# Kernel optimization log

Hardware: AMD Instinct MI355X
Metric: run time of the kernel (lower is better)

The kernel has to match this reference:

```python
import jax, jax.numpy as jnp
import numpy as np


def setup_inputs() -> dict:
    key = jax.random.key(0)
    B, N, D = 4, 8192, 16
    inputs = jax.random.normal(key, (B, N, D), dtype=jnp.float32)
    return {"inputs": inputs, "k": 16}


def reference(inputs, k):
    # pairwise squared distances: ||x_i||^2 - 2 x_i.x_j + ||x_j||^2  -> [B, N, N]
    inner = -2.0 * jnp.einsum("bnd,bmd->bnm", inputs, inputs)
    square = jnp.sum(inputs * inputs, axis=-1, keepdims=True)  # [B, N, 1]
    adj = square + inner + jnp.swapaxes(square, 1, 2)          # [B, N, N]
    # k smallest distances -> top-k of negated matrix
    _, nn_idx = jax.lax.top_k(-adj, k)                          # [B, N, k]
    return nn_idx
```

## Files before the change

kernel.cpp:

```cpp
#include <hip/hip_runtime.h>


#define B_    4
#define N_    8192
#define D_    16
#define K_    16
#define SEGS_ 8
#define SEG_  (N_ / SEGS_)
#define CH_   8
#define NCH_  (SEG_ / CH_)
#define BT_   512
#define CAP_  12
#define NQ_   (B_ * N_)

typedef unsigned long long u64;
typedef float v2f __attribute__((ext_vector_type(2)));

__device__ __forceinline__ v2f pk_fma(v2f a, v2f b, v2f c) {
  v2f d;
  asm("v_pk_fma_f32 %0, %1, %2, %3" : "=v"(d) : "v"(a), "v"(b), "v"(c));
  return d;
}
__device__ __forceinline__ v2f pk_mul(v2f a, v2f b) {
  v2f d;
  asm("v_pk_mul_f32 %0, %1, %2" : "=v"(d) : "v"(a), "v"(b));
  return d;
}
__device__ __forceinline__ v2f pk_add(v2f a, v2f b) {
  v2f d;
  asm("v_pk_add_f32 %0, %1, %2" : "=v"(d) : "v"(a), "v"(b));
  return d;
}

__device__ __forceinline__ float np_norm16(const float* __restrict__ p) {
#pragma clang fp contract(off)
  float m[16];
#pragma unroll
  for (int d = 0; d < 16; ++d) m[d] = p[d] * p[d];
  float r[8];
#pragma unroll
  for (int j = 0; j < 8; ++j) r[j] = m[j] + m[j + 8];
  float q[4];
#pragma unroll
  for (int j = 0; j < 4; ++j) q[j] = r[j] + r[j + 4];
  return (q[0] + q[2]) + (q[1] + q[3]);
}

__device__ __forceinline__ unsigned mono32(float f) {
  unsigned u = __float_as_uint(f);
  return u ^ ((unsigned)((int)u >> 31) | 0x80000000u);
}

__global__ __launch_bounds__(256) void knn_norms(const float* __restrict__ x,
                                                 float* __restrict__ nrm) {
  int q = blockIdx.x * 256 + threadIdx.x;
  float row[16];
  const float4* xv = (const float4*)(x + (size_t)q * D_);
  float4 a = xv[0], b = xv[1], c = xv[2], d = xv[3];
  row[0]=a.x; row[1]=a.y; row[2]=a.z; row[3]=a.w;
  row[4]=b.x; row[5]=b.y; row[6]=b.z; row[7]=b.w;
  row[8]=c.x; row[9]=c.y; row[10]=c.z; row[11]=c.w;
  row[12]=d.x; row[13]=d.y; row[14]=d.z; row[15]=d.w;
  nrm[q] = np_norm16(row);
}

__device__ __forceinline__ void insert16(float d, int j, float (&kd)[K_], int (&ki)[K_]) {
  float cd = d; int ci = j;
#pragma unroll
  for (int p = 0; p < K_; ++p) {
    bool gt = kd[p] > cd;
    float t0 = gt ? cd : kd[p];
    float t1 = gt ? kd[p] : cd;
    int   t2 = gt ? ci : ki[p];
    int   t3 = gt ? ki[p] : ci;
    kd[p] = t0; cd = t1; ki[p] = t2; ci = t3;
  }
}

__device__ __forceinline__ void flushbuf(u64* __restrict__ pbuf, int tid,
                                         int& count, float& thr,
                                         float (&kd)[K_], int (&ki)[K_]) {
#pragma unroll 1
  for (int s = 0; s < CAP_; ++s) {
    if (s < count) {
      u64 e = pbuf[s * BT_ + tid];
      float d = __uint_as_float((unsigned)(e >> 32));
      if (d < thr) {
        int j = (int)(e & 0xffffu);
        insert16(d, j, kd, ki);
        thr = kd[K_ - 1];
      }
    }
  }
  count = 0;
}

__global__ __launch_bounds__(BT_, 2) void knn_fused(const float* __restrict__ x,
                                                    const float* __restrict__ nrm,
                                                    int* __restrict__ out) {
  __shared__ u64 smem[7232];
  v2f*    stageT = (v2f*)smem;
  float*  stageN = (float*)(smem + 1024);
  u64*    pbuf   = smem + 1088;

  const int tid  = threadIdx.x;
  const int w    = tid >> 6;
  const int lane = tid & 63;
  const int q    = blockIdx.x * 64 + lane;
  const int bq   = (int)((blockIdx.x * 64u) >> 13);
  const int row0 = bq * N_ + w * SEG_;
  const float* __restrict__ cbase = x + (size_t)row0 * D_;
  const float* __restrict__ nbase = nrm + row0;

  const int p_ = lane >> 4;
  const int d_ = lane & 15;

  v2f qq[D_];
  {
    const float4* qv = (const float4*)(x + (size_t)q * D_);
    float4 v0 = qv[0], v1 = qv[1], v2 = qv[2], v3 = qv[3];
    qq[0]=(v2f){v0.x,v0.x}; qq[1]=(v2f){v0.y,v0.y}; qq[2]=(v2f){v0.z,v0.z}; qq[3]=(v2f){v0.w,v0.w};
    qq[4]=(v2f){v1.x,v1.x}; qq[5]=(v2f){v1.y,v1.y}; qq[6]=(v2f){v1.z,v1.z}; qq[7]=(v2f){v1.w,v1.w};
    qq[8]=(v2f){v2.x,v2.x}; qq[9]=(v2f){v2.y,v2.y}; qq[10]=(v2f){v2.z,v2.z}; qq[11]=(v2f){v2.w,v2.w};
    qq[12]=(v2f){v3.x,v3.x}; qq[13]=(v2f){v3.y,v3.y}; qq[14]=(v2f){v3.z,v3.z}; qq[15]=(v2f){v3.w,v3.w};
  }
  const float ni = nrm[q];
  const v2f nip = (v2f){ni, ni};
  const v2f m2  = (v2f){-2.0f, -2.0f};

  float kd[K_]; int ki[K_];
#pragma unroll
  for (int p = 0; p < K_; ++p) { kd[p] = 3.4e38f; ki[p] = 0; }
  float thr = 3.4e38f;
  int count = 0;

  {
    float g0 = cbase[(2 * p_) * D_ + d_];
    float g1 = cbase[(2 * p_ + 1) * D_ + d_];
    stageT[(w * 2 + 0) * 64 + p_ * 16 + d_] = (v2f){g0, g1};
    if (lane < CH_) stageN[(w * 2 + 0) * CH_ + lane] = nbase[lane];
  }

#pragma unroll 1
  for (int c = 0; c < NCH_; ++c) {
    const int b = c & 1;
    float pg0 = 0.f, pg1 = 0.f, pn = 0.f;
    const bool more = (c + 1 < NCH_);
    if (more) {
      const float* cb = cbase + (size_t)(c + 1) * CH_ * D_;
      pg0 = cb[(2 * p_) * D_ + d_];
      pg1 = cb[(2 * p_ + 1) * D_ + d_];
      if (lane < CH_) pn = nbase[(c + 1) * CH_ + lane];
    }

    const float4* tp = (const float4*)(stageT + (w * 2 + b) * 64);
    const float*  nW = stageN + (w * 2 + b) * CH_;
    const int j0 = c * CH_;

#pragma unroll 1
    for (int p = 0; p < 4; ++p) {
      float4 f0 = tp[p*8+0], f1 = tp[p*8+1], f2 = tp[p*8+2], f3 = tp[p*8+3];
      float4 f4 = tp[p*8+4], f5 = tp[p*8+5], f6 = tp[p*8+6], f7 = tp[p*8+7];

      v2f acc = (v2f){0.f, 0.f};
      acc = pk_fma(qq[0],  (v2f){f0.x, f0.y}, acc);
      acc = pk_fma(qq[1],  (v2f){f0.z, f0.w}, acc);
      acc = pk_fma(qq[2],  (v2f){f1.x, f1.y}, acc);
      acc = pk_fma(qq[3],  (v2f){f1.z, f1.w}, acc);
      acc = pk_fma(qq[4],  (v2f){f2.x, f2.y}, acc);
      acc = pk_fma(qq[5],  (v2f){f2.z, f2.w}, acc);
      acc = pk_fma(qq[6],  (v2f){f3.x, f3.y}, acc);
      acc = pk_fma(qq[7],  (v2f){f3.z, f3.w}, acc);
      acc = pk_fma(qq[8],  (v2f){f4.x, f4.y}, acc);
      acc = pk_fma(qq[9],  (v2f){f4.z, f4.w}, acc);
      acc = pk_fma(qq[10], (v2f){f5.x, f5.y}, acc);
      acc = pk_fma(qq[11], (v2f){f5.z, f5.w}, acc);
      acc = pk_fma(qq[12], (v2f){f6.x, f6.y}, acc);
      acc = pk_fma(qq[13], (v2f){f6.z, f6.w}, acc);
      acc = pk_fma(qq[14], (v2f){f7.x, f7.y}, acc);
      acc = pk_fma(qq[15], (v2f){f7.z, f7.w}, acc);

      v2f ii  = pk_mul(m2, acc);
      v2f uu  = pk_add(nip, ii);
      v2f njp = *(const v2f*)(nW + 2 * p);
      v2f dd  = pk_add(uu, njp);
      float d0 = dd.x, d1 = dd.y;
      const int j = j0 + 2 * p;

      if (d0 < thr) {
        pbuf[count * BT_ + tid] = ((u64)__float_as_uint(d0) << 32) | (unsigned)j;
        ++count;
      }
      if (d1 < thr) {
        pbuf[count * BT_ + tid] = ((u64)__float_as_uint(d1) << 32) | (unsigned)(j + 1);
        ++count;
      }
      if (__any(count >= CAP_ - 1)) flushbuf(pbuf, tid, count, thr, kd, ki);
    }

    if (more) {
      stageT[(w * 2 + (b ^ 1)) * 64 + p_ * 16 + d_] = (v2f){pg0, pg1};
      if (lane < CH_) stageN[(w * 2 + (b ^ 1)) * CH_ + lane] = pn;
    }
  }
  flushbuf(pbuf, tid, count, thr, kd, ki);

  u64* mrg = smem + 1088;
  const int half = lane >> 5;
  const int lm   = lane & 31;

  __syncthreads();
#pragma unroll 1
  for (int h = 0; h < 2; ++h) {
    if (half == h) {
#pragma unroll
      for (int p = 0; p < K_; ++p) {
        mrg[((size_t)w * 16 + p) * 32 + lm] =
            ((u64)mono32(kd[p]) << 32) | (unsigned)(w * SEG_ + ki[p]);
      }
    }
    __syncthreads();

    if (tid < 256) {
      const int m  = tid >> 3;
      const int s  = tid & 7;
      const int qi = h * 32 + m;
      const int gq = blockIdx.x * 64 + qi;
      int ptr = 0;
#pragma unroll 1
      for (int r = 0; r < K_; ++r) {
        u64 hd = mrg[((size_t)s * 16 + ptr) * 32 + m];
        u64 mv = hd, o;
        o = __shfl_xor(mv, 1); mv = (o < mv) ? o : mv;
        o = __shfl_xor(mv, 2); mv = (o < mv) ? o : mv;
        o = __shfl_xor(mv, 4); mv = (o < mv) ? o : mv;
        if (hd == mv) ++ptr;
        if (s == 0) out[(size_t)gq * K_ + r] = (int)(mv & 0xffffu);
      }
    }
    __syncthreads();
  }
}

extern "C" void kernel_launch(void* const* d_in, const int* in_sizes, int n_in,
                              void* d_out, int out_size, void* d_ws, size_t ws_size,
                              hipStream_t stream) {
  const float* x = (const float*)d_in[0];
  float* nrm = (float*)d_ws;
  int* out = (int*)d_out;

  knn_norms<<<NQ_ / 256, 256, 0, stream>>>(x, nrm);
  knn_fused<<<NQ_ / 64, BT_, 0, stream>>>(x, nrm, out);
}
```

Before: 333.9 us.

## Process two queries per thread to reuse staged candidate tiles

Each thread now handles two query points (128 per block instead of 64), so each candidate tile loaded from LDS feeds two sets of packed FMAs. Each query keeps its own top-k state, candidate buffer and flush path, and the final merge runs four times. The aim is to halve LDS and staging traffic per distance computed and to add independent FMA chains for latency hiding. In exchange register pressure roughly doubles, launch bounds drop to one block per SM, LDS use nearly doubles, and there are half as many blocks.

```diff
diff --git a/kernel.cpp b/kernel.cpp
--- a/kernel.cpp
+++ b/kernel.cpp
@@ -12,6 +12,7 @@
 #define BT_   512
 #define CAP_  12
 #define NQ_   (B_ * N_)
+#define QB_   128
 
 typedef unsigned long long u64;
 typedef float v2f __attribute__((ext_vector_type(2)));
@@ -95,19 +96,52 @@
   count = 0;
 }
 
-__global__ __launch_bounds__(BT_, 2) void knn_fused(const float* __restrict__ x,
+__device__ __forceinline__ void pub_merge(u64* __restrict__ mrg,
+                                          const float (&kd)[K_], const int (&ki)[K_],
+                                          int w, int lane, int tid, int hl,
+                                          int qbase, int* __restrict__ out) {
+  if ((lane >> 5) == hl) {
+    const int lm = lane & 31;
+#pragma unroll
+    for (int p = 0; p < K_; ++p) {
+      mrg[((size_t)w * 16 + p) * 32 + lm] =
+          ((u64)mono32(kd[p]) << 32) | (unsigned)(w * SEG_ + ki[p]);
+    }
+  }
+  __syncthreads();
+  if (tid < 256) {
+    const int m = tid >> 3;
+    const int s = tid & 7;
+    int ptr = 0;
+#pragma unroll 1
+    for (int r = 0; r < K_; ++r) {
+      u64 hd = mrg[((size_t)s * 16 + ptr) * 32 + m];
+      u64 mv = hd, o;
+      o = __shfl_xor(mv, 1); mv = (o < mv) ? o : mv;
+      o = __shfl_xor(mv, 2); mv = (o < mv) ? o : mv;
+      o = __shfl_xor(mv, 4); mv = (o < mv) ? o : mv;
+      if (hd == mv) ++ptr;
+      if (s == 0) out[(size_t)(qbase + m) * K_ + r] = (int)(mv & 0xffffu);
+    }
+  }
+  __syncthreads();
+}
+
+__global__ __launch_bounds__(BT_, 1) void knn_fused(const float* __restrict__ x,
                                                     const float* __restrict__ nrm,
                                                     int* __restrict__ out) {
-  __shared__ u64 smem[7232];
+  __shared__ u64 smem[13376];
   v2f*    stageT = (v2f*)smem;
   float*  stageN = (float*)(smem + 1024);
-  u64*    pbuf   = smem + 1088;
+  u64*    pbufA  = smem + 1088;
+  u64*    pbufB  = smem + 7232;
 
   const int tid  = threadIdx.x;
   const int w    = tid >> 6;
   const int lane = tid & 63;
-  const int q    = blockIdx.x * 64 + lane;
-  const int bq   = (int)((blockIdx.x * 64u) >> 13);
+  const int q0   = blockIdx.x * QB_ + lane;
+  const int q1   = q0 + 64;
+  const int bq   = (int)((blockIdx.x * (unsigned)QB_) >> 13);
   const int row0 = bq * N_ + w * SEG_;
   const float* __restrict__ cbase = x + (size_t)row0 * D_;
   const float* __restrict__ nbase = nrm + row0;
@@ -115,24 +149,36 @@
   const int p_ = lane >> 4;
   const int d_ = lane & 15;
 
-  v2f qq[D_];
+  v2f qqA[D_], qqB[D_];
   {
-    const float4* qv = (const float4*)(x + (size_t)q * D_);
+    const float4* qv = (const float4*)(x + (size_t)q0 * D_);
     float4 v0 = qv[0], v1 = qv[1], v2 = qv[2], v3 = qv[3];
-    qq[0]=(v2f){v0.x,v0.x}; qq[1]=(v2f){v0.y,v0.y}; qq[2]=(v2f){v0.z,v0.z}; qq[3]=(v2f){v0.w,v0.w};
-    qq[4]=(v2f){v1.x,v1.x}; qq[5]=(v2f){v1.y,v1.y}; qq[6]=(v2f){v1.z,v1.z}; qq[7]=(v2f){v1.w,v1.w};
-    qq[8]=(v2f){v2.x,v2.x}; qq[9]=(v2f){v2.y,v2.y}; qq[10]=(v2f){v2.z,v2.z}; qq[11]=(v2f){v2.w,v2.w};
-    qq[12]=(v2f){v3.x,v3.x}; qq[13]=(v2f){v3.y,v3.y}; qq[14]=(v2f){v3.z,v3.z}; qq[15]=(v2f){v3.w,v3.w};
-  }
-  const float ni = nrm[q];
-  const v2f nip = (v2f){ni, ni};
-  const v2f m2  = (v2f){-2.0f, -2.0f};
-
-  float kd[K_]; int ki[K_];
-#pragma unroll
-  for (int p = 0; p < K_; ++p) { kd[p] = 3.4e38f; ki[p] = 0; }
-  float thr = 3.4e38f;
-  int count = 0;
+    qqA[0]=(v2f){v0.x,v0.x}; qqA[1]=(v2f){v0.y,v0.y}; qqA[2]=(v2f){v0.z,v0.z}; qqA[3]=(v2f){v0.w,v0.w};
+    qqA[4]=(v2f){v1.x,v1.x}; qqA[5]=(v2f){v1.y,v1.y}; qqA[6]=(v2f){v1.z,v1.z}; qqA[7]=(v2f){v1.w,v1.w};
+    qqA[8]=(v2f){v2.x,v2.x}; qqA[9]=(v2f){v2.y,v2.y}; qqA[10]=(v2f){v2.z,v2.z}; qqA[11]=(v2f){v2.w,v2.w};
+    qqA[12]=(v2f){v3.x,v3.x}; qqA[13]=(v2f){v3.y,v3.y}; qqA[14]=(v2f){v3.z,v3.z}; qqA[15]=(v2f){v3.w,v3.w};
+  }
+  {
+    const float4* qv = (const float4*)(x + (size_t)q1 * D_);
+    float4 v0 = qv[0], v1 = qv[1], v2 = qv[2], v3 = qv[3];
+    qqB[0]=(v2f){v0.x,v0.x}; qqB[1]=(v2f){v0.y,v0.y}; qqB[2]=(v2f){v0.z,v0.z}; qqB[3]=(v2f){v0.w,v0.w};
+    qqB[4]=(v2f){v1.x,v1.x}; qqB[5]=(v2f){v1.y,v1.y}; qqB[6]=(v2f){v1.z,v1.z}; qqB[7]=(v2f){v1.w,v1.w};
+    qqB[8]=(v2f){v2.x,v2.x}; qqB[9]=(v2f){v2.y,v2.y}; qqB[10]=(v2f){v2.z,v2.z}; qqB[11]=(v2f){v2.w,v2.w};
+    qqB[12]=(v2f){v3.x,v3.x}; qqB[13]=(v2f){v3.y,v3.y}; qqB[14]=(v2f){v3.z,v3.z}; qqB[15]=(v2f){v3.w,v3.w};
+  }
+  const float niA = nrm[q0], niB = nrm[q1];
+  const v2f nipA = (v2f){niA, niA};
+  const v2f nipB = (v2f){niB, niB};
+  const v2f m2   = (v2f){-2.0f, -2.0f};
+
+  float kdA[K_], kdB[K_]; int kiA[K_], kiB[K_];
+#pragma unroll
+  for (int p = 0; p < K_; ++p) {
+    kdA[p] = 3.4e38f; kiA[p] = 0;
+    kdB[p] = 3.4e38f; kiB[p] = 0;
+  }
+  float thrA = 3.4e38f, thrB = 3.4e38f;
+  int cntA = 0, cntB = 0;
 
   {
     float g0 = cbase[(2 * p_) * D_ + d_];
@@ -162,40 +208,67 @@
       float4 f0 = tp[p*8+0], f1 = tp[p*8+1], f2 = tp[p*8+2], f3 = tp[p*8+3];
       float4 f4 = tp[p*8+4], f5 = tp[p*8+5], f6 = tp[p*8+6], f7 = tp[p*8+7];
 
-      v2f acc = (v2f){0.f, 0.f};
-      acc = pk_fma(qq[0],  (v2f){f0.x, f0.y}, acc);
-      acc = pk_fma(qq[1],  (v2f){f0.z, f0.w}, acc);
-      acc = pk_fma(qq[2],  (v2f){f1.x, f1.y}, acc);
-      acc = pk_fma(qq[3],  (v2f){f1.z, f1.w}, acc);
-      acc = pk_fma(qq[4],  (v2f){f2.x, f2.y}, acc);
-      acc = pk_fma(qq[5],  (v2f){f2.z, f2.w}, acc);
-      acc = pk_fma(qq[6],  (v2f){f3.x, f3.y}, acc);
-      acc = pk_fma(qq[7],  (v2f){f3.z, f3.w}, acc);
-      acc = pk_fma(qq[8],  (v2f){f4.x, f4.y}, acc);
-      acc = pk_fma(qq[9],  (v2f){f4.z, f4.w}, acc);
-      acc = pk_fma(qq[10], (v2f){f5.x, f5.y}, acc);
-      acc = pk_fma(qq[11], (v2f){f5.z, f5.w}, acc);
-      acc = pk_fma(qq[12], (v2f){f6.x, f6.y}, acc);
-      acc = pk_fma(qq[13], (v2f){f6.z, f6.w}, acc);
-      acc = pk_fma(qq[14], (v2f){f7.x, f7.y}, acc);
-      acc = pk_fma(qq[15], (v2f){f7.z, f7.w}, acc);
-
-      v2f ii  = pk_mul(m2, acc);
-      v2f uu  = pk_add(nip, ii);
+      v2f accA = (v2f){0.f, 0.f}, accB = (v2f){0.f, 0.f};
+      accA = pk_fma(qqA[0],  (v2f){f0.x, f0.y}, accA);
+      accB = pk_fma(qqB[0],  (v2f){f0.x, f0.y}, accB);
+      accA = pk_fma(qqA[1],  (v2f){f0.z, f0.w}, accA);
+      accB = pk_fma(qqB[1],  (v2f){f0.z, f0.w}, accB);
+      accA = pk_fma(qqA[2],  (v2f){f1.x, f1.y}, accA);
+      accB = pk_fma(qqB[2],  (v2f){f1.x, f1.y}, accB);
+      accA = pk_fma(qqA[3],  (v2f){f1.z, f1.w}, accA);
+      accB = pk_fma(qqB[3],  (v2f){f1.z, f1.w}, accB);
+      accA = pk_fma(qqA[4],  (v2f){f2.x, f2.y}, accA);
+      accB = pk_fma(qqB[4],  (v2f){f2.x, f2.y}, accB);
+      accA = pk_fma(qqA[5],  (v2f){f2.z, f2.w}, accA);
+      accB = pk_fma(qqB[5],  (v2f){f2.z, f2.w}, accB);
+      accA = pk_fma(qqA[6],  (v2f){f3.x, f3.y}, accA);
+      accB = pk_fma(qqB[6],  (v2f){f3.x, f3.y}, accB);
+      accA = pk_fma(qqA[7],  (v2f){f3.z, f3.w}, accA);
+      accB = pk_fma(qqB[7],  (v2f){f3.z, f3.w}, accB);
+      accA = pk_fma(qqA[8],  (v2f){f4.x, f4.y}, accA);
+      accB = pk_fma(qqB[8],  (v2f){f4.x, f4.y}, accB);
+      accA = pk_fma(qqA[9],  (v2f){f4.z, f4.w}, accA);
+      accB = pk_fma(qqB[9],  (v2f){f4.z, f4.w}, accB);
+      accA = pk_fma(qqA[10], (v2f){f5.x, f5.y}, accA);
+      accB = pk_fma(qqB[10], (v2f){f5.x, f5.y}, accB);
+      accA = pk_fma(qqA[11], (v2f){f5.z, f5.w}, accA);
+      accB = pk_fma(qqB[11], (v2f){f5.z, f5.w}, accB);
+      accA = pk_fma(qqA[12], (v2f){f6.x, f6.y}, accA);
+      accB = pk_fma(qqB[12], (v2f){f6.x, f6.y}, accB);
+      accA = pk_fma(qqA[13], (v2f){f6.z, f6.w}, accA);
+      accB = pk_fma(qqB[13], (v2f){f6.z, f6.w}, accB);
+      accA = pk_fma(qqA[14], (v2f){f7.x, f7.y}, accA);
+      accB = pk_fma(qqB[14], (v2f){f7.x, f7.y}, accB);
+      accA = pk_fma(qqA[15], (v2f){f7.z, f7.w}, accA);
+      accB = pk_fma(qqB[15], (v2f){f7.z, f7.w}, accB);
+
       v2f njp = *(const v2f*)(nW + 2 * p);
-      v2f dd  = pk_add(uu, njp);
-      float d0 = dd.x, d1 = dd.y;
+      v2f iA  = pk_mul(m2, accA);
+      v2f iB  = pk_mul(m2, accB);
+      v2f uA  = pk_add(nipA, iA);
+      v2f uB  = pk_add(nipB, iB);
+      v2f dA  = pk_add(uA, njp);
+      v2f dB  = pk_add(uB, njp);
       const int j = j0 + 2 * p;
 
-      if (d0 < thr) {
-        pbuf[count * BT_ + tid] = ((u64)__float_as_uint(d0) << 32) | (unsigned)j;
-        ++count;
-      }
-      if (d1 < thr) {
-        pbuf[count * BT_ + tid] = ((u64)__float_as_uint(d1) << 32) | (unsigned)(j + 1);
-        ++count;
-      }
-      if (__any(count >= CAP_ - 1)) flushbuf(pbuf, tid, count, thr, kd, ki);
+      if (dA.x < thrA) {
+        pbufA[cntA * BT_ + tid] = ((u64)__float_as_uint(dA.x) << 32) | (unsigned)j;
+        ++cntA;
+      }
+      if (dA.y < thrA) {
+        pbufA[cntA * BT_ + tid] = ((u64)__float_as_uint(dA.y) << 32) | (unsigned)(j + 1);
+        ++cntA;
+      }
+      if (dB.x < thrB) {
+        pbufB[cntB * BT_ + tid] = ((u64)__float_as_uint(dB.x) << 32) | (unsigned)j;
+        ++cntB;
+      }
+      if (dB.y < thrB) {
+        pbufB[cntB * BT_ + tid] = ((u64)__float_as_uint(dB.y) << 32) | (unsigned)(j + 1);
+        ++cntB;
+      }
+      if (__any(cntA >= CAP_ - 1)) flushbuf(pbufA, tid, cntA, thrA, kdA, kiA);
+      if (__any(cntB >= CAP_ - 1)) flushbuf(pbufB, tid, cntB, thrB, kdB, kiB);
     }
 
     if (more) {
@@ -203,43 +276,16 @@
       if (lane < CH_) stageN[(w * 2 + (b ^ 1)) * CH_ + lane] = pn;
     }
   }
-  flushbuf(pbuf, tid, count, thr, kd, ki);
+  flushbuf(pbufA, tid, cntA, thrA, kdA, kiA);
+  flushbuf(pbufB, tid, cntB, thrB, kdB, kiB);
 
   u64* mrg = smem + 1088;
-  const int half = lane >> 5;
-  const int lm   = lane & 31;
-
   __syncthreads();
-#pragma unroll 1
-  for (int h = 0; h < 2; ++h) {
-    if (half == h) {
-#pragma unroll
-      for (int p = 0; p < K_; ++p) {
-        mrg[((size_t)w * 16 + p) * 32 + lm] =
-            ((u64)mono32(kd[p]) << 32) | (unsigned)(w * SEG_ + ki[p]);
-      }
-    }
-    __syncthreads();
-
-    if (tid < 256) {
-      const int m  = tid >> 3;
-      const int s  = tid & 7;
-      const int qi = h * 32 + m;
-      const int gq = blockIdx.x * 64 + qi;
-      int ptr = 0;
-#pragma unroll 1
-      for (int r = 0; r < K_; ++r) {
-        u64 hd = mrg[((size_t)s * 16 + ptr) * 32 + m];
-        u64 mv = hd, o;
-        o = __shfl_xor(mv, 1); mv = (o < mv) ? o : mv;
-        o = __shfl_xor(mv, 2); mv = (o < mv) ? o : mv;
-        o = __shfl_xor(mv, 4); mv = (o < mv) ? o : mv;
-        if (hd == mv) ++ptr;
-        if (s == 0) out[(size_t)gq * K_ + r] = (int)(mv & 0xffffu);
-      }
-    }
-    __syncthreads();
-  }
+  const int qb = blockIdx.x * QB_;
+  pub_merge(mrg, kdA, kiA, w, lane, tid, 0, qb +  0, out);
+  pub_merge(mrg, kdA, kiA, w, lane, tid, 1, qb + 32, out);
+  pub_merge(mrg, kdB, kiB, w, lane, tid, 0, qb + 64, out);
+  pub_merge(mrg, kdB, kiB, w, lane, tid, 1, qb + 96, out);
 }
 
 extern "C" void kernel_launch(void* const* d_in, const int* in_sizes, int n_in,
@@ -250,5 +296,5 @@
   int* out = (int*)d_out;
 
   knn_norms<<<NQ_ / 256, 256, 0, stream>>>(x, nrm);
-  knn_fused<<<NQ_ / 64, BT_, 0, stream>>>(x, nrm, out);
-}
+  knn_fused<<<NQ_ / QB_, BT_, 0, stream>>>(x, nrm, out);
+}
```

After: 414.7 us. +24.2%, slower.

## Split candidate pairs across wave halves, halve queries per block, branchless buffer append

Applied to the files above, without the earlier changes.

Each block now handles 32 queries instead of 64. The two halves of each wave process alternating candidate pairs for the same query, which doubles the number of parallel top-k streams, and the final merge becomes a 16-way shuffle reduction. The candidate buffer capacity drops and shared memory shrinks so the launch bound can target 4 blocks per CU. Appends are now unconditional stores with a predicated count increment, which removes branch divergence. In exchange, every query's row is loaded and its norm computed twice, and flushes may happen more often because the buffer is smaller.

```diff
diff --git a/kernel.cpp b/kernel.cpp
--- a/kernel.cpp
+++ b/kernel.cpp
@@ -10,8 +10,9 @@
 #define CH_   8
 #define NCH_  (SEG_ / CH_)
 #define BT_   512
-#define CAP_  12
+#define CAP_  7
 #define NQ_   (B_ * N_)
+#define QB_   32
 
 typedef unsigned long long u64;
 typedef float v2f __attribute__((ext_vector_type(2)));
@@ -95,10 +96,10 @@
   count = 0;
 }
 
-__global__ __launch_bounds__(BT_, 2) void knn_fused(const float* __restrict__ x,
+__global__ __launch_bounds__(BT_, 4) void knn_fused(const float* __restrict__ x,
                                                     const float* __restrict__ nrm,
                                                     int* __restrict__ out) {
-  __shared__ u64 smem[7232];
+  __shared__ u64 smem[4672];
   v2f*    stageT = (v2f*)smem;
   float*  stageN = (float*)(smem + 1024);
   u64*    pbuf   = smem + 1088;
@@ -106,8 +107,10 @@
   const int tid  = threadIdx.x;
   const int w    = tid >> 6;
   const int lane = tid & 63;
-  const int q    = blockIdx.x * 64 + lane;
-  const int bq   = (int)((blockIdx.x * 64u) >> 13);
+  const int h    = lane >> 5;
+  const int ql   = lane & 31;
+  const int q    = blockIdx.x * QB_ + ql;
+  const int bq   = (int)((blockIdx.x * (unsigned)QB_) >> 13);
   const int row0 = bq * N_ + w * SEG_;
   const float* __restrict__ cbase = x + (size_t)row0 * D_;
   const float* __restrict__ nbase = nrm + row0;
@@ -158,9 +161,10 @@
     const int j0 = c * CH_;
 
 #pragma unroll 1
-    for (int p = 0; p < 4; ++p) {
-      float4 f0 = tp[p*8+0], f1 = tp[p*8+1], f2 = tp[p*8+2], f3 = tp[p*8+3];
-      float4 f4 = tp[p*8+4], f5 = tp[p*8+5], f6 = tp[p*8+6], f7 = tp[p*8+7];
+    for (int t = 0; t < 2; ++t) {
+      const int pr = 2 * t + h;
+      float4 f0 = tp[pr*8+0], f1 = tp[pr*8+1], f2 = tp[pr*8+2], f3 = tp[pr*8+3];
+      float4 f4 = tp[pr*8+4], f5 = tp[pr*8+5], f6 = tp[pr*8+6], f7 = tp[pr*8+7];
 
       v2f acc = (v2f){0.f, 0.f};
       acc = pk_fma(qq[0],  (v2f){f0.x, f0.y}, acc);
@@ -180,21 +184,19 @@
       acc = pk_fma(qq[14], (v2f){f7.x, f7.y}, acc);
       acc = pk_fma(qq[15], (v2f){f7.z, f7.w}, acc);
 
+      v2f njp = *(const v2f*)(nW + 2 * pr);
       v2f ii  = pk_mul(m2, acc);
       v2f uu  = pk_add(nip, ii);
-      v2f njp = *(const v2f*)(nW + 2 * p);
       v2f dd  = pk_add(uu, njp);
-      float d0 = dd.x, d1 = dd.y;
-      const int j = j0 + 2 * p;
-
-      if (d0 < thr) {
-        pbuf[count * BT_ + tid] = ((u64)__float_as_uint(d0) << 32) | (unsigned)j;
-        ++count;
-      }
-      if (d1 < thr) {
-        pbuf[count * BT_ + tid] = ((u64)__float_as_uint(d1) << 32) | (unsigned)(j + 1);
-        ++count;
-      }
+      const int j = j0 + 2 * pr;
+
+      pbuf[count * BT_ + tid] =
+          ((u64)__float_as_uint(dd.x) << 32) | (unsigned)j;
+      count += (dd.x < thr) ? 1 : 0;
+      pbuf[count * BT_ + tid] =
+          ((u64)__float_as_uint(dd.y) << 32) | (unsigned)(j + 1);
+      count += (dd.y < thr) ? 1 : 0;
+
       if (__any(count >= CAP_ - 1)) flushbuf(pbuf, tid, count, thr, kd, ki);
     }
 
@@ -205,37 +207,37 @@
   }
   flushbuf(pbuf, tid, count, thr, kd, ki);
 
-  u64* mrg = smem + 1088;
-  const int half = lane >> 5;
-  const int lm   = lane & 31;
-
+  u64* mrg = smem;
+  const int strm = w * 2 + h;
   __syncthreads();
 #pragma unroll 1
-  for (int h = 0; h < 2; ++h) {
-    if (half == h) {
+  for (int P = 0; P < 2; ++P) {
+    if ((ql >> 4) == P) {
+      const int m = ql & 15;
 #pragma unroll
       for (int p = 0; p < K_; ++p) {
-        mrg[((size_t)w * 16 + p) * 32 + lm] =
+        mrg[((size_t)strm * 16 + p) * 16 + m] =
             ((u64)mono32(kd[p]) << 32) | (unsigned)(w * SEG_ + ki[p]);
       }
     }
     __syncthreads();
 
     if (tid < 256) {
-      const int m  = tid >> 3;
-      const int s  = tid & 7;
-      const int qi = h * 32 + m;
-      const int gq = blockIdx.x * 64 + qi;
+      const int m = tid >> 4;
+      const int s = tid & 15;
       int ptr = 0;
 #pragma unroll 1
       for (int r = 0; r < K_; ++r) {
-        u64 hd = mrg[((size_t)s * 16 + ptr) * 32 + m];
+        u64 hd = mrg[((size_t)s * 16 + ptr) * 16 + m];
         u64 mv = hd, o;
         o = __shfl_xor(mv, 1); mv = (o < mv) ? o : mv;
         o = __shfl_xor(mv, 2); mv = (o < mv) ? o : mv;
         o = __shfl_xor(mv, 4); mv = (o < mv) ? o : mv;
+        o = __shfl_xor(mv, 8); mv = (o < mv) ? o : mv;
         if (hd == mv) ++ptr;
-        if (s == 0) out[(size_t)gq * K_ + r] = (int)(mv & 0xffffu);
+        if (s == 0)
+          out[(size_t)(blockIdx.x * QB_ + P * 16 + m) * K_ + r] =
+              (int)(mv & 0xffffu);
       }
     }
     __syncthreads();
@@ -250,5 +252,5 @@
   int* out = (int*)d_out;
 
   knn_norms<<<NQ_ / 256, 256, 0, stream>>>(x, nrm);
-  knn_fused<<<NQ_ / 64, BT_, 0, stream>>>(x, nrm, out);
-}
+  knn_fused<<<NQ_ / QB_, BT_, 0, stream>>>(x, nrm, out);
+}
```

Measured after the change: 439.9 us. 31.8% more time.
